# Kernel tuning notes

Hardware: AMD Instinct MI355X
Metric: run time of the kernel (lower is better)

The kernel has to match this reference:

```python
import jax, jax.numpy as jnp
import numpy as np

B, N, CC, CF, H, W = 4, 4, 256, 512, 128, 128
h, w = H // 2, W // 2


def _upsample2x(x):
    return jnp.repeat(jnp.repeat(x, 2, axis=2), 2, axis=3)


def setup_inputs() -> dict:
    key = jax.random.key(0)
    ks = jax.random.split(key, 8)
    return {
        "contexts": jax.random.normal(ks[0], (B, N, CC, H, W), dtype=jnp.float32),
        "mainstream": jax.random.normal(ks[1], (B, CF, h, w), dtype=jnp.float32),
        "Wc_w": jax.random.normal(ks[2], (CC, CC), dtype=jnp.float32) * 0.02,  # 1x1 conv Cc->Cc
        "Wc_b": jnp.zeros((CC,), dtype=jnp.float32),
        "Wf_w": jax.random.normal(ks[3], (CC, CF), dtype=jnp.float32) * 0.02,  # 1x1 conv Cf->Cc
        "Wf_b": jnp.zeros((CC,), dtype=jnp.float32),
        "Wv_w": jax.random.normal(ks[4], (CC, CF, 3, 3), dtype=jnp.float32) * 0.02,  # 3x3 conv Cf->Cc
        "Wv_b": jnp.zeros((CC,), dtype=jnp.float32),
    }


def reference(contexts, mainstream, Wc_w, Wc_b, Wf_w, Wf_b, Wv_w, Wv_b):
    # queries: 1x1 conv Cf->Cc on mainstream  [B,Cc,h,w]
    queries = jnp.einsum('oc,bchw->bohw', Wf_w, mainstream) + Wf_b[None, :, None, None]
    # keys: 1x1 conv Cc->Cc applied to every context  [B,N,Cc,H,W]
    keys = jnp.einsum('oc,bnchw->bnohw', Wc_w, contexts) + Wc_b[None, None, :, None, None]
    # values: 3x3 conv Cf->Cc, padding 1  [B,Cc,h,w]
    values = jax.lax.conv_general_dilated(
        mainstream, Wv_w, window_strides=(1, 1), padding='SAME',
        dimension_numbers=('NCHW', 'OIHW', 'NCHW')) + Wv_b[None, :, None, None]
    q_up = _upsample2x(queries)   # [B,Cc,H,W]
    v_up = _upsample2x(values)    # [B,Cc,H,W]
    # per-pixel attention scores over the N contexts
    scores = jnp.einsum('bnchw,bchw->bnhw', keys, q_up)      # [B,N,H,W]
    attn = jax.nn.softmax(scores, axis=1)                    # softmax over contexts
    attn_out = jnp.einsum('bnchw,bnhw->bchw', contexts, attn)
    return attn_out + v_up
```

## Files before the change

### kernel.cpp

```cpp
#include <hip/hip_runtime.h>

#define NB   4
#define NN   4
#define CCh  256
#define CFh  512
#define HH   128
#define WW   128
#define PLO  4096
#define PHI  16384

typedef __bf16 bf16;
typedef __bf16 bf16x8 __attribute__((ext_vector_type(8)));
typedef float  f32x4  __attribute__((ext_vector_type(4)));
typedef float  f32x2  __attribute__((ext_vector_type(2)));

__device__ __forceinline__ void gll16(const void* g, void* lds) {
    __builtin_amdgcn_global_load_lds(
        (const __attribute__((address_space(1))) void*)g,
        (__attribute__((address_space(3))) void*)lds, 16, 0, 0);
}

__device__ __forceinline__ unsigned pack2bf(float a, float b) {
    unsigned short ua = __builtin_bit_cast(unsigned short, (bf16)a);
    unsigned short ub = __builtin_bit_cast(unsigned short, (bf16)b);
    return (unsigned)ua | ((unsigned)ub << 16);
}

__global__ void prep_mqk(const float* __restrict__ Wc_w, const float* __restrict__ Wf_w,
                         const float* __restrict__ Wf_b, bf16* __restrict__ M_qk,
                         float* __restrict__ d_qk) {
    __shared__ float red[256];
    int c = blockIdx.y;
    int f = blockIdx.x * 256 + threadIdx.x;
    float s = 0.f;
#pragma unroll 8
    for (int o = 0; o < CCh; ++o)
        s += Wc_w[o * CCh + c] * Wf_w[o * CFh + f];
    M_qk[c * CFh + f] = (bf16)s;
    if (blockIdx.x == 0) {
        int o = threadIdx.x;
        red[o] = Wc_w[o * CCh + c] * Wf_b[o];
        __syncthreads();
        for (int st = 128; st > 0; st >>= 1) {
            if (threadIdx.x < st) red[threadIdx.x] += red[threadIdx.x + st];
            __syncthreads();
        }
        if (threadIdx.x == 0) d_qk[c] = red[0];
    }
}

__global__ void prep_ms(const float* __restrict__ ms, bf16* __restrict__ ms_t) {
    __shared__ float tile[32][33];
    int b = blockIdx.z;
    int p0 = blockIdx.x * 32, f0 = blockIdx.y * 32;
    int tx = threadIdx.x;
    int r = tx >> 5, cc = tx & 31;
    const float* src = ms + (size_t)b * CFh * PLO;
#pragma unroll
    for (int q = 0; q < 4; ++q) {
        int fl = q * 8 + r;
        tile[fl][cc] = src[(size_t)(f0 + fl) * PLO + p0 + cc];
    }
    __syncthreads();
    bf16* dst = ms_t + (size_t)b * PLO * CFh;
    int fp = tx & 15;
    int r2 = tx >> 4;
#pragma unroll
    for (int q = 0; q < 2; ++q) {
        int pl = q * 16 + r2;
        unsigned w = pack2bf(tile[2 * fp][pl], tile[2 * fp + 1][pl]);
        *((unsigned*)(dst + (size_t)(p0 + pl) * CFh + f0) + fp) = w;
    }
}

__global__ void prep_wv(const float* __restrict__ Wv_w, bf16* __restrict__ Wv_p,
                        bf16* __restrict__ zerob) {
    int tid = blockIdx.x * 256 + threadIdx.x;
    int t = tid / (CCh * CFh);
    int rem = tid % (CCh * CFh);
    int c = rem / CFh, f = rem % CFh;
    Wv_p[tid] = (bf16)Wv_w[(size_t)(c * CFh + f) * 9 + t];
    if (tid < 1024) zerob[tid] = (bf16)0.f;
}

__global__ __launch_bounds__(256) void gemm_kernel(
    const bf16* __restrict__ Wv_p,
    const bf16* __restrict__ M_qk,
    const bf16* __restrict__ ms_t,
    const float* __restrict__ d_qk,
    const bf16* __restrict__ zerob,
    float* __restrict__ v3, bf16* __restrict__ qk_out) {
    __shared__ __align__(16) bf16 Alds[128 * 32];
    __shared__ __align__(16) bf16 Blds[128 * 32];

    const int tx = threadIdx.x;
    const int wave = tx >> 6, lane = tx & 63;
    const int ptile = blockIdx.x, ctile = blockIdx.y;
    const int z = blockIdx.z;
    const int mode = (z >= 12);
    const int b = mode ? (z - 12) : (z / 3);
    const int tg = mode ? 0 : (z % 3);
    const int t0 = tg * 3;
    const int ntaps = mode ? 1 : 3;

    const bf16* Wbase = mode ? M_qk : (Wv_p + (size_t)t0 * CCh * CFh);
    const bf16* msb = ms_t + (size_t)b * PLO * CFh;

    int idx0 = wave * 2048 + lane * 16;
    int idx1 = idx0 + 1024;
    int rA0 = idx0 >> 6, fq0 = (idx0 >> 4) & 3;
    int rA1 = idx1 >> 6, fq1 = (idx1 >> 4) & 3;
    const size_t aoff0 = (size_t)(ctile * 128 + rA0) * CFh + fq0 * 8;
    const size_t aoff1 = (size_t)(ctile * 128 + rA1) * CFh + fq1 * 8;
    char* ldsA0 = (char*)Alds + wave * 2048;
    char* ldsA1 = ldsA0 + 1024;
    char* ldsB0 = (char*)Blds + wave * 2048;
    char* ldsB1 = ldsB0 + 1024;

    const int p0 = ptile * 128 + rA0, p1 = ptile * 128 + rA1;
    const int i0 = p0 >> 6, j0 = p0 & 63;
    const int i1 = p1 >> 6, j1 = p1 & 63;

    f32x4 acc[4][4];
#pragma unroll
    for (int mi = 0; mi < 4; ++mi)
#pragma unroll
        for (int ni = 0; ni < 4; ++ni) acc[mi][ni] = f32x4{0.f, 0.f, 0.f, 0.f};

    const int wm = wave >> 1, wn = wave & 1;
    const int quad = lane >> 4, l15 = lane & 15;

    for (int t = 0; t < ntaps; ++t) {
        const int dy = mode ? 0 : ((t0 + t) / 3 - 1);
        const int dx = mode ? 0 : ((t0 + t) % 3 - 1);
        const bf16* Wt = Wbase + (size_t)t * CCh * CFh;
        int si0 = i0 + dy, sj0 = j0 + dx, si1 = i1 + dy, sj1 = j1 + dx;
        bool ok0 = (unsigned)si0 < 64u && (unsigned)sj0 < 64u;
        bool ok1 = (unsigned)si1 < 64u && (unsigned)sj1 < 64u;
        const bf16* bsrc0 = ok0 ? msb + (size_t)(si0 * 64 + sj0) * CFh + fq0 * 8 : zerob;
        const bf16* bsrc1 = ok1 ? msb + (size_t)(si1 * 64 + sj1) * CFh + fq1 * 8 : zerob;

        for (int fc = 0; fc < CFh / 32; ++fc) {
            const int f0 = fc * 32;
            __syncthreads();
            gll16(Wt + aoff0 + f0, ldsA0);
            gll16(Wt + aoff1 + f0, ldsA1);
            gll16(bsrc0 + f0, ldsB0);
            gll16(bsrc1 + f0, ldsB1);
            __syncthreads();

            bf16x8 af[4], bfr[4];
#pragma unroll
            for (int mi = 0; mi < 4; ++mi)
                af[mi] = *(const bf16x8*)&Alds[(wm * 64 + mi * 16 + l15) * 32 + quad * 8];
#pragma unroll
            for (int ni = 0; ni < 4; ++ni)
                bfr[ni] = *(const bf16x8*)&Blds[(wn * 64 + ni * 16 + l15) * 32 + quad * 8];
#pragma unroll
            for (int mi = 0; mi < 4; ++mi)
#pragma unroll
                for (int ni = 0; ni < 4; ++ni)
                    acc[mi][ni] = __builtin_amdgcn_mfma_f32_16x16x32_bf16(
                        af[mi], bfr[ni], acc[mi][ni], 0, 0, 0);
        }
    }

    if (mode) {
        bf16* obase = qk_out + (size_t)b * CCh * PLO;
#pragma unroll
        for (int mi = 0; mi < 4; ++mi) {
            int cb = ctile * 128 + wm * 64 + mi * 16 + quad * 4;
#pragma unroll
            for (int ni = 0; ni < 4; ++ni) {
                int p = ptile * 128 + wn * 64 + ni * 16 + l15;
                bf16* op = obase + (size_t)cb * PLO + p;
#pragma unroll
                for (int r = 0; r < 4; ++r)
                    op[(size_t)r * PLO] = (bf16)(acc[mi][ni][r] + d_qk[cb + r]);
            }
        }
    } else {
        float* obase = v3 + (size_t)(tg * NB + b) * CCh * PLO;
#pragma unroll
        for (int mi = 0; mi < 4; ++mi) {
            int cb = ctile * 128 + wm * 64 + mi * 16 + quad * 4;
#pragma unroll
            for (int ni = 0; ni < 4; ++ni) {
                int p = ptile * 128 + wn * 64 + ni * 16 + l15;
                float* op = obase + (size_t)cb * PLO + p;
#pragma unroll
                for (int r = 0; r < 4; ++r)
                    op[(size_t)r * PLO] = acc[mi][ni][r];
            }
        }
    }
}

__global__ __launch_bounds__(512) void attn_kernel(
    const float* __restrict__ ctx,
    const bf16* __restrict__ qk,
    const float* __restrict__ v3,
    const float* __restrict__ Wv_b,
    float* __restrict__ out) {
    __shared__ f32x4 swred[4][8][16];
    const int tx = threadIdx.x;
    const int pq = tx & 15;
    const int cc = tx >> 4;
    const int lane = tx & 63;
    const int wv = tx >> 6;
    const int quad = lane >> 4;

    const int pbase = blockIdx.x << 6;
    const int b = pbase >> 14;
    const int rem = pbase & 16383;
    const int hh = rem >> 7;
    const int w0 = rem & 127;
    const int wq = w0 + pq * 4;
    const int i = hh >> 1, j0 = wq >> 1;

    const int c0 = cc * 8;
    const size_t NSTR = (size_t)CCh * PHI;
    const float* cbase = ctx + (size_t)b * NN * NSTR + (size_t)c0 * PHI
                             + (size_t)hh * WW + wq;
    const bf16* qkb = qk + ((size_t)b * CCh + c0) * PLO + i * 64 + j0;
    const float* vbp = v3 + ((size_t)b * CCh + c0) * PLO + i * 64 + j0;

    f32x4 vals[4][8];
    f32x4 s[4];
#pragma unroll
    for (int n = 0; n < 4; ++n) s[n] = f32x4{0.f, 0.f, 0.f, 0.f};

#pragma unroll
    for (int cj = 0; cj < 8; ++cj) {
        unsigned qw = *(const unsigned*)(qkb + (size_t)cj * PLO);
        float qa = __uint_as_float(qw << 16);
        float qb = __uint_as_float(qw & 0xffff0000u);
        f32x4 qv = {qa, qa, qb, qb};
#pragma unroll
        for (int n = 0; n < 4; ++n) {
            vals[n][cj] = *(const f32x4*)(cbase + n * NSTR + (size_t)cj * PHI);
            s[n] += vals[n][cj] * qv;
        }
    }
#pragma unroll
    for (int n = 0; n < 4; ++n) {
#pragma unroll
        for (int m = 16; m <= 32; m <<= 1) {
            f32x4 t;
            t[0] = __shfl_xor(s[n][0], m);
            t[1] = __shfl_xor(s[n][1], m);
            t[2] = __shfl_xor(s[n][2], m);
            t[3] = __shfl_xor(s[n][3], m);
            s[n] += t;
        }
    }
    f32x4 sq = (quad == 0) ? s[0] : (quad == 1) ? s[1] : (quad == 2) ? s[2] : s[3];
    swred[quad][wv][pq] = sq;
    __syncthreads();

    f32x4 t4[4];
#pragma unroll
    for (int n = 0; n < 4; ++n) {
        f32x4 a = swred[n][0][pq];
#pragma unroll
        for (int w = 1; w < 8; ++w) a += swred[n][w][pq];
        t4[n] = a;
    }
    f32x4 mx;
#pragma unroll
    for (int k = 0; k < 4; ++k)
        mx[k] = fmaxf(fmaxf(t4[0][k], t4[1][k]), fmaxf(t4[2][k], t4[3][k]));
    f32x4 e[4];
#pragma unroll
    for (int n = 0; n < 4; ++n)
#pragma unroll
        for (int k = 0; k < 4; ++k) e[n][k] = __expf(t4[n][k] - mx[k]);
    f32x4 ssum = e[0] + e[1] + e[2] + e[3];
    f32x4 a4[4];
#pragma unroll
    for (int n = 0; n < 4; ++n)
#pragma unroll
        for (int k = 0; k < 4; ++k) a4[n][k] = e[n][k] / ssum[k];

    float* outp = out + ((size_t)b * CCh + c0) * PHI + (size_t)hh * WW + wq;
#pragma unroll
    for (int cj = 0; cj < 8; ++cj) {
        f32x2 vv = *(const f32x2*)(vbp + (size_t)cj * PLO);
        vv += *(const f32x2*)(vbp + 4194304 + (size_t)cj * PLO);
        vv += *(const f32x2*)(vbp + 8388608 + (size_t)cj * PLO);
        float bc = Wv_b[c0 + cj];
        float va = vv[0] + bc, vb2 = vv[1] + bc;
        f32x4 o = vals[0][cj] * a4[0] + vals[1][cj] * a4[1] +
                  vals[2][cj] * a4[2] + vals[3][cj] * a4[3] +
                  f32x4{va, va, vb2, vb2};
        *(f32x4*)(outp + (size_t)cj * PHI) = o;
    }
}

extern "C" void kernel_launch(void* const* d_in, const int* in_sizes, int n_in,
                              void* d_out, int out_size, void* d_ws, size_t ws_size,
                              hipStream_t stream) {
    const float* ctx  = (const float*)d_in[0];
    const float* ms   = (const float*)d_in[1];
    const float* Wc_w = (const float*)d_in[2];
    const float* Wf_w = (const float*)d_in[4];
    const float* Wf_b = (const float*)d_in[5];
    const float* Wv_w = (const float*)d_in[6];
    const float* Wv_b = (const float*)d_in[7];
    float* out = (float*)d_out;

    char* ws = (char*)d_ws;
    bf16*  ms_t  = (bf16*)ws;
    bf16*  Wv_p  = (bf16*)(ws + 16777216);
    bf16*  M_qk  = (bf16*)(ws + 19136512);
    float* d_qk  = (float*)(ws + 19398656);
    bf16*  zerob = (bf16*)(ws + 19399680);
    bf16*  qk    = (bf16*)(ws + 19401728);
    float* v3    = (float*)(ws + 27790336);

    prep_mqk<<<dim3(2, 256), 256, 0, stream>>>(Wc_w, Wf_w, Wf_b, M_qk, d_qk);
    prep_ms<<<dim3(128, 16, 4), 256, 0, stream>>>(ms, ms_t);
    prep_wv<<<dim3(4608), 256, 0, stream>>>(Wv_w, Wv_p, zerob);
    gemm_kernel<<<dim3(32, 2, 16), 256, 0, stream>>>(Wv_p, M_qk, ms_t, d_qk,
                                                     zerob, v3, qk);
    attn_kernel<<<dim3(1024), 512, 0, stream>>>(ctx, qk, v3, Wv_b, out);
}
```

Before: 503.3 us.

## Double-buffer LDS tiles in the MFMA GEMM to overlap loads with compute

The nested tap and channel-chunk loops are flattened into a single iteration loop over double-buffered LDS tiles. The next chunk's global-to-LDS loads are issued before computing on the current buffer, using explicit vmcnt waits and barriers. This hides global memory latency behind MFMA work, at the cost of twice the LDS footprint and hand-managed waitcnt ordering that must stay correct.

Result: slower. 513.7 us (+2.1%).

```diff
diff --git a/kernel.cpp b/kernel.cpp
--- a/kernel.cpp
+++ b/kernel.cpp
@@ -90,8 +90,8 @@
     const float* __restrict__ d_qk,
     const bf16* __restrict__ zerob,
     float* __restrict__ v3, bf16* __restrict__ qk_out) {
-    __shared__ __align__(16) bf16 Alds[128 * 32];
-    __shared__ __align__(16) bf16 Blds[128 * 32];
+    __shared__ __align__(16) bf16 Alds[2][128 * 32];
+    __shared__ __align__(16) bf16 Blds[2][128 * 32];
 
     const int tx = threadIdx.x;
     const int wave = tx >> 6, lane = tx & 63;
@@ -101,7 +101,7 @@
     const int b = mode ? (z - 12) : (z / 3);
     const int tg = mode ? 0 : (z % 3);
     const int t0 = tg * 3;
-    const int ntaps = mode ? 1 : 3;
+    const int NIT = mode ? 16 : 48;
 
     const bf16* Wbase = mode ? M_qk : (Wv_p + (size_t)t0 * CCh * CFh);
     const bf16* msb = ms_t + (size_t)b * PLO * CFh;
@@ -112,10 +112,6 @@
     int rA1 = idx1 >> 6, fq1 = (idx1 >> 4) & 3;
     const size_t aoff0 = (size_t)(ctile * 128 + rA0) * CFh + fq0 * 8;
     const size_t aoff1 = (size_t)(ctile * 128 + rA1) * CFh + fq1 * 8;
-    char* ldsA0 = (char*)Alds + wave * 2048;
-    char* ldsA1 = ldsA0 + 1024;
-    char* ldsB0 = (char*)Blds + wave * 2048;
-    char* ldsB1 = ldsB0 + 1024;
 
     const int p0 = ptile * 128 + rA0, p1 = ptile * 128 + rA1;
     const int i0 = p0 >> 6, j0 = p0 & 63;
@@ -130,40 +126,72 @@
     const int wm = wave >> 1, wn = wave & 1;
     const int quad = lane >> 4, l15 = lane & 15;
 
-    for (int t = 0; t < ntaps; ++t) {
-        const int dy = mode ? 0 : ((t0 + t) / 3 - 1);
-        const int dx = mode ? 0 : ((t0 + t) % 3 - 1);
-        const bf16* Wt = Wbase + (size_t)t * CCh * CFh;
-        int si0 = i0 + dy, sj0 = j0 + dx, si1 = i1 + dy, sj1 = j1 + dx;
-        bool ok0 = (unsigned)si0 < 64u && (unsigned)sj0 < 64u;
-        bool ok1 = (unsigned)si1 < 64u && (unsigned)sj1 < 64u;
-        const bf16* bsrc0 = ok0 ? msb + (size_t)(si0 * 64 + sj0) * CFh + fq0 * 8 : zerob;
-        const bf16* bsrc1 = ok1 ? msb + (size_t)(si1 * 64 + sj1) * CFh + fq1 * 8 : zerob;
-
-        for (int fc = 0; fc < CFh / 32; ++fc) {
-            const int f0 = fc * 32;
-            __syncthreads();
-            gll16(Wt + aoff0 + f0, ldsA0);
-            gll16(Wt + aoff1 + f0, ldsA1);
-            gll16(bsrc0 + f0, ldsB0);
-            gll16(bsrc1 + f0, ldsB1);
-            __syncthreads();
-
-            bf16x8 af[4], bfr[4];
-#pragma unroll
-            for (int mi = 0; mi < 4; ++mi)
-                af[mi] = *(const bf16x8*)&Alds[(wm * 64 + mi * 16 + l15) * 32 + quad * 8];
+    const bf16* bsrc0; const bf16* bsrc1; const bf16* Wt;
+#define SET_TAP(tt) do {                                                        \
+        int t_ = (tt);                                                          \
+        int dy = mode ? 0 : ((t0 + t_) / 3 - 1);                                \
+        int dx = mode ? 0 : ((t0 + t_) % 3 - 1);                                \
+        int si0 = i0 + dy, sj0 = j0 + dx, si1 = i1 + dy, sj1 = j1 + dx;         \
+        bsrc0 = ((unsigned)si0 < 64u && (unsigned)sj0 < 64u)                    \
+                    ? msb + (size_t)(si0 * 64 + sj0) * CFh + fq0 * 8 : zerob;   \
+        bsrc1 = ((unsigned)si1 < 64u && (unsigned)sj1 < 64u)                    \
+                    ? msb + (size_t)(si1 * 64 + sj1) * CFh + fq1 * 8 : zerob;   \
+        Wt = Wbase + (size_t)t_ * CCh * CFh;                                    \
+    } while (0)
+
+    SET_TAP(0);
+    {
+        char* lA = (char*)(&Alds[0][0]) + wave * 2048;
+        char* lB = (char*)(&Blds[0][0]) + wave * 2048;
+        gll16(Wt + aoff0, lA);
+        gll16(Wt + aoff1, lA + 1024);
+        gll16(bsrc0, lB);
+        gll16(bsrc1, lB + 1024);
+    }
+    asm volatile("s_waitcnt vmcnt(0)" ::: "memory");
+    __builtin_amdgcn_s_barrier();
+    asm volatile("" ::: "memory");
+
+    for (int it = 0; it < NIT; ++it) {
+        const int buf = it & 1;
+        const int nx = it + 1;
+        if (nx < NIT) {
+            if ((nx & 15) == 0) SET_TAP(nx >> 4);
+            const int fo = (nx & 15) * 32;
+            char* lA = (char*)(&Alds[buf ^ 1][0]) + wave * 2048;
+            char* lB = (char*)(&Blds[buf ^ 1][0]) + wave * 2048;
+            gll16(Wt + aoff0 + fo, lA);
+            gll16(Wt + aoff1 + fo, lA + 1024);
+            gll16(bsrc0 + fo, lB);
+            gll16(bsrc1 + fo, lB + 1024);
+            asm volatile("s_waitcnt vmcnt(4)" ::: "memory");
+        } else {
+            asm volatile("s_waitcnt vmcnt(0)" ::: "memory");
+        }
+        __builtin_amdgcn_s_barrier();
+        asm volatile("" ::: "memory");
+
+        const bf16* Ab = &Alds[buf][0];
+        const bf16* Bb = &Blds[buf][0];
+        bf16x8 af[4], bfr[4];
+#pragma unroll
+        for (int mi = 0; mi < 4; ++mi)
+            af[mi] = *(const bf16x8*)&Ab[(wm * 64 + mi * 16 + l15) * 32 + quad * 8];
+#pragma unroll
+        for (int ni = 0; ni < 4; ++ni)
+            bfr[ni] = *(const bf16x8*)&Bb[(wn * 64 + ni * 16 + l15) * 32 + quad * 8];
+#pragma unroll
+        for (int mi = 0; mi < 4; ++mi)
 #pragma unroll
             for (int ni = 0; ni < 4; ++ni)
-                bfr[ni] = *(const bf16x8*)&Blds[(wn * 64 + ni * 16 + l15) * 32 + quad * 8];
-#pragma unroll
-            for (int mi = 0; mi < 4; ++mi)
-#pragma unroll
-                for (int ni = 0; ni < 4; ++ni)
-                    acc[mi][ni] = __builtin_amdgcn_mfma_f32_16x16x32_bf16(
-                        af[mi], bfr[ni], acc[mi][ni], 0, 0, 0);
-        }
-    }
+                acc[mi][ni] = __builtin_amdgcn_mfma_f32_16x16x32_bf16(
+                    af[mi], bfr[ni], acc[mi][ni], 0, 0, 0);
+
+        asm volatile("" ::: "memory");
+        __builtin_amdgcn_s_barrier();
+        asm volatile("" ::: "memory");
+    }
+#undef SET_TAP
 
     if (mode) {
         bf16* obase = qk_out + (size_t)b * CCh * PLO;
```

## Pad mainstream into halo grid and share B tile across three horizontal taps

Applied to the files above, without the earlier changes.

The transposed mainstream is now stored in a zero-padded 66x72 grid per batch, so conv taps need no bounds checks or zero buffer. The GEMM loads a two-row-plus-halo B strip once per K chunk and reuses it for all three dx taps by shifting the LDS read offset. The three tap weight tiles are loaded together, which cuts the number of barriers and global B reloads. The three prep kernels are merged into one launch, plus a memset of the padded buffer, at the cost of more LDS and extra memset traffic.

After: 491.5 us. 2.3% less time.

```diff
diff --git a/kernel.cpp b/kernel.cpp
--- a/kernel.cpp
+++ b/kernel.cpp
@@ -8,6 +8,9 @@
 #define WW   128
 #define PLO  4096
 #define PHI  16384
+#define GR   66
+#define GC   72
+#define PLANE_E (GR * GC * CFh)
 
 typedef __bf16 bf16;
 typedef __bf16 bf16x8 __attribute__((ext_vector_type(8)));
@@ -26,72 +29,71 @@
     return (unsigned)ua | ((unsigned)ub << 16);
 }
 
-__global__ void prep_mqk(const float* __restrict__ Wc_w, const float* __restrict__ Wf_w,
-                         const float* __restrict__ Wf_b, bf16* __restrict__ M_qk,
-                         float* __restrict__ d_qk) {
+__global__ void prep_fused(const float* __restrict__ Wc_w, const float* __restrict__ Wf_w,
+                           const float* __restrict__ Wf_b, const float* __restrict__ ms,
+                           const float* __restrict__ Wv_w,
+                           bf16* __restrict__ M_qk, float* __restrict__ d_qk,
+                           bf16* __restrict__ msg, bf16* __restrict__ Wv_p) {
     __shared__ float red[256];
-    int c = blockIdx.y;
-    int f = blockIdx.x * 256 + threadIdx.x;
-    float s = 0.f;
+    __shared__ float tile[32][33];
+    const int bid = blockIdx.x, tx = threadIdx.x;
+
+    if (bid < 512) {
+        int c = bid >> 1;
+        int f = (bid & 1) * 256 + tx;
+        float s = 0.f;
 #pragma unroll 8
-    for (int o = 0; o < CCh; ++o)
-        s += Wc_w[o * CCh + c] * Wf_w[o * CFh + f];
-    M_qk[c * CFh + f] = (bf16)s;
-    if (blockIdx.x == 0) {
-        int o = threadIdx.x;
-        red[o] = Wc_w[o * CCh + c] * Wf_b[o];
+        for (int o = 0; o < CCh; ++o)
+            s += Wc_w[o * CCh + c] * Wf_w[o * CFh + f];
+        M_qk[c * CFh + f] = (bf16)s;
+        if ((bid & 1) == 0) {
+            red[tx] = Wc_w[tx * CCh + c] * Wf_b[tx];
+            __syncthreads();
+            for (int st = 128; st > 0; st >>= 1) {
+                if (tx < st) red[tx] += red[tx + st];
+                __syncthreads();
+            }
+            if (tx == 0) d_qk[c] = red[0];
+        }
+    } else if (bid < 5120) {
+        int tid = (bid - 512) * 256 + tx;
+        int t = tid / (CCh * CFh);
+        int rem = tid % (CCh * CFh);
+        int c = rem / CFh, f = rem % CFh;
+        Wv_p[tid] = (bf16)Wv_w[(size_t)(c * CFh + f) * 9 + t];
+    } else {
+        int id2 = bid - 5120;
+        int x = id2 & 127, y = (id2 >> 7) & 15, b = id2 >> 11;
+        int p0 = x * 32, f0 = y * 32;
+        int r = tx >> 5, cc = tx & 31;
+        const float* src = ms + (size_t)b * CFh * PLO;
+#pragma unroll
+        for (int q = 0; q < 4; ++q) {
+            int fl = q * 8 + r;
+            tile[fl][cc] = src[(size_t)(f0 + fl) * PLO + p0 + cc];
+        }
         __syncthreads();
-        for (int st = 128; st > 0; st >>= 1) {
-            if (threadIdx.x < st) red[threadIdx.x] += red[threadIdx.x + st];
-            __syncthreads();
-        }
-        if (threadIdx.x == 0) d_qk[c] = red[0];
-    }
-}
-
-__global__ void prep_ms(const float* __restrict__ ms, bf16* __restrict__ ms_t) {
-    __shared__ float tile[32][33];
-    int b = blockIdx.z;
-    int p0 = blockIdx.x * 32, f0 = blockIdx.y * 32;
-    int tx = threadIdx.x;
-    int r = tx >> 5, cc = tx & 31;
-    const float* src = ms + (size_t)b * CFh * PLO;
-#pragma unroll
-    for (int q = 0; q < 4; ++q) {
-        int fl = q * 8 + r;
-        tile[fl][cc] = src[(size_t)(f0 + fl) * PLO + p0 + cc];
-    }
-    __syncthreads();
-    bf16* dst = ms_t + (size_t)b * PLO * CFh;
-    int fp = tx & 15;
-    int r2 = tx >> 4;
-#pragma unroll
-    for (int q = 0; q < 2; ++q) {
-        int pl = q * 16 + r2;
-        unsigned w = pack2bf(tile[2 * fp][pl], tile[2 * fp + 1][pl]);
-        *((unsigned*)(dst + (size_t)(p0 + pl) * CFh + f0) + fp) = w;
-    }
-}
-
-__global__ void prep_wv(const float* __restrict__ Wv_w, bf16* __restrict__ Wv_p,
-                        bf16* __restrict__ zerob) {
-    int tid = blockIdx.x * 256 + threadIdx.x;
-    int t = tid / (CCh * CFh);
-    int rem = tid % (CCh * CFh);
-    int c = rem / CFh, f = rem % CFh;
-    Wv_p[tid] = (bf16)Wv_w[(size_t)(c * CFh + f) * 9 + t];
-    if (tid < 1024) zerob[tid] = (bf16)0.f;
+        bf16* dstb = msg + (size_t)b * PLANE_E;
+        int fp = tx & 15, r2 = tx >> 4;
+#pragma unroll
+        for (int q = 0; q < 2; ++q) {
+            int pl = q * 16 + r2;
+            int pix = p0 + pl;
+            int pi = pix >> 6, pj = pix & 63;
+            unsigned w = pack2bf(tile[2 * fp][pl], tile[2 * fp + 1][pl]);
+            *((unsigned*)(dstb + ((size_t)(pi + 1) * GC + pj + 1) * CFh + f0) + fp) = w;
+        }
+    }
 }
 
 __global__ __launch_bounds__(256) void gemm_kernel(
     const bf16* __restrict__ Wv_p,
     const bf16* __restrict__ M_qk,
-    const bf16* __restrict__ ms_t,
+    const bf16* __restrict__ msg,
     const float* __restrict__ d_qk,
-    const bf16* __restrict__ zerob,
     float* __restrict__ v3, bf16* __restrict__ qk_out) {
-    __shared__ __align__(16) bf16 Alds[128 * 32];
-    __shared__ __align__(16) bf16 Blds[128 * 32];
+    __shared__ __align__(16) bf16 Alds[3 * 128 * 32];
+    __shared__ __align__(16) bf16 Blds[2 * GC * 32];
 
     const int tx = threadIdx.x;
     const int wave = tx >> 6, lane = tx & 63;
@@ -100,26 +102,30 @@
     const int mode = (z >= 12);
     const int b = mode ? (z - 12) : (z / 3);
     const int tg = mode ? 0 : (z % 3);
-    const int t0 = tg * 3;
+    const int dy = mode ? 0 : (tg - 1);
     const int ntaps = mode ? 1 : 3;
 
-    const bf16* Wbase = mode ? M_qk : (Wv_p + (size_t)t0 * CCh * CFh);
-    const bf16* msb = ms_t + (size_t)b * PLO * CFh;
-
-    int idx0 = wave * 2048 + lane * 16;
-    int idx1 = idx0 + 1024;
-    int rA0 = idx0 >> 6, fq0 = (idx0 >> 4) & 3;
-    int rA1 = idx1 >> 6, fq1 = (idx1 >> 4) & 3;
-    const size_t aoff0 = (size_t)(ctile * 128 + rA0) * CFh + fq0 * 8;
-    const size_t aoff1 = (size_t)(ctile * 128 + rA1) * CFh + fq1 * 8;
-    char* ldsA0 = (char*)Alds + wave * 2048;
-    char* ldsA1 = ldsA0 + 1024;
-    char* ldsB0 = (char*)Blds + wave * 2048;
-    char* ldsB1 = ldsB0 + 1024;
-
-    const int p0 = ptile * 128 + rA0, p1 = ptile * 128 + rA1;
-    const int i0 = p0 >> 6, j0 = p0 & 63;
-    const int i1 = p1 >> 6, j1 = p1 & 63;
+    const bf16* Wbase = mode ? M_qk : (Wv_p + (size_t)tg * 3 * CCh * CFh);
+    const bf16* msb = msg + (size_t)b * PLANE_E;
+    const int i0 = ptile * 2;
+
+    int aoffs[6];
+#pragma unroll
+    for (int k = 0; k < 6; ++k) {
+        int q = wave + 4 * k;
+        int tap = q >> 3, s = q & 7;
+        aoffs[k] = tap * (CCh * CFh) + (ctile * 128 + s * 16 + (lane >> 2)) * CFh
+                 + (lane & 3) * 8;
+    }
+    int boffs[3];
+#pragma unroll
+    for (int k = 0; k < 3; ++k) {
+        int q = wave + 4 * k;
+        int cfl = q * 16 + (lane >> 2);
+        int ri = (cfl >= GC) ? 1 : 0;
+        int jj = cfl - GC * ri;
+        boffs[k] = ((i0 + ri + dy + 1) * GC + jj) * CFh + (lane & 3) * 8;
+    }
 
     f32x4 acc[4][4];
 #pragma unroll
@@ -129,33 +135,35 @@
 
     const int wm = wave >> 1, wn = wave & 1;
     const int quad = lane >> 4, l15 = lane & 15;
-
-    for (int t = 0; t < ntaps; ++t) {
-        const int dy = mode ? 0 : ((t0 + t) / 3 - 1);
-        const int dx = mode ? 0 : ((t0 + t) % 3 - 1);
-        const bf16* Wt = Wbase + (size_t)t * CCh * CFh;
-        int si0 = i0 + dy, sj0 = j0 + dx, si1 = i1 + dy, sj1 = j1 + dx;
-        bool ok0 = (unsigned)si0 < 64u && (unsigned)sj0 < 64u;
-        bool ok1 = (unsigned)si1 < 64u && (unsigned)sj1 < 64u;
-        const bf16* bsrc0 = ok0 ? msb + (size_t)(si0 * 64 + sj0) * CFh + fq0 * 8 : zerob;
-        const bf16* bsrc1 = ok1 ? msb + (size_t)(si1 * 64 + sj1) * CFh + fq1 * 8 : zerob;
-
-        for (int fc = 0; fc < CFh / 32; ++fc) {
-            const int f0 = fc * 32;
-            __syncthreads();
-            gll16(Wt + aoff0 + f0, ldsA0);
-            gll16(Wt + aoff1 + f0, ldsA1);
-            gll16(bsrc0 + f0, ldsB0);
-            gll16(bsrc1 + f0, ldsB1);
-            __syncthreads();
-
+    const int nA = ntaps * 2;
+
+    for (int fc = 0; fc < 16; ++fc) {
+        const int f0 = fc * 32;
+        __syncthreads();
+#pragma unroll
+        for (int k = 0; k < 6; ++k)
+            if (k < nA)
+                gll16(Wbase + aoffs[k] + f0, (char*)Alds + (wave + 4 * k) * 1024);
+#pragma unroll
+        for (int k = 0; k < 3; ++k)
+            if (wave + 4 * k < 9)
+                gll16(msb + boffs[k] + f0, (char*)Blds + (wave + 4 * k) * 1024);
+        __syncthreads();
+
+        for (int t = 0; t < ntaps; ++t) {
+            const int dxo = mode ? 1 : t;
             bf16x8 af[4], bfr[4];
 #pragma unroll
             for (int mi = 0; mi < 4; ++mi)
-                af[mi] = *(const bf16x8*)&Alds[(wm * 64 + mi * 16 + l15) * 32 + quad * 8];
-#pragma unroll
-            for (int ni = 0; ni < 4; ++ni)
-                bfr[ni] = *(const bf16x8*)&Blds[(wn * 64 + ni * 16 + l15) * 32 + quad * 8];
+                af[mi] = *(const bf16x8*)((const char*)Alds + t * 8192 +
+                          (wm * 64 + mi * 16 + l15) * 64 + quad * 16);
+#pragma unroll
+            for (int ni = 0; ni < 4; ++ni) {
+                int pl = wn * 64 + ni * 16 + l15;
+                int ri = pl >> 6, j = pl & 63;
+                bfr[ni] = *(const bf16x8*)((const char*)Blds +
+                           (ri * GC + j + dxo) * 64 + quad * 16);
+            }
 #pragma unroll
             for (int mi = 0; mi < 4; ++mi)
 #pragma unroll
@@ -310,18 +318,16 @@
     float* out = (float*)d_out;
 
     char* ws = (char*)d_ws;
-    bf16*  ms_t  = (bf16*)ws;
-    bf16*  Wv_p  = (bf16*)(ws + 16777216);
-    bf16*  M_qk  = (bf16*)(ws + 19136512);
-    float* d_qk  = (float*)(ws + 19398656);
-    bf16*  zerob = (bf16*)(ws + 19399680);
-    bf16*  qk    = (bf16*)(ws + 19401728);
-    float* v3    = (float*)(ws + 27790336);
-
-    prep_mqk<<<dim3(2, 256), 256, 0, stream>>>(Wc_w, Wf_w, Wf_b, M_qk, d_qk);
-    prep_ms<<<dim3(128, 16, 4), 256, 0, stream>>>(ms, ms_t);
-    prep_wv<<<dim3(4608), 256, 0, stream>>>(Wv_w, Wv_p, zerob);
-    gemm_kernel<<<dim3(32, 2, 16), 256, 0, stream>>>(Wv_p, M_qk, ms_t, d_qk,
-                                                     zerob, v3, qk);
+    bf16*  msg  = (bf16*)ws;
+    bf16*  Wv_p = (bf16*)(ws + 19464192);
+    bf16*  M_qk = (bf16*)(ws + 21823488);
+    float* d_qk = (float*)(ws + 22085632);
+    bf16*  qk   = (bf16*)(ws + 22086656);
+    float* v3   = (float*)(ws + 30475264);
+
+    hipMemsetAsync(msg, 0, 19464192, stream);
+    prep_fused<<<dim3(13312), 256, 0, stream>>>(Wc_w, Wf_w, Wf_b, ms, Wv_w,
+                                                M_qk, d_qk, msg, Wv_p);
+    gemm_kernel<<<dim3(32, 2, 16), 256, 0, stream>>>(Wv_p, M_qk, msg, d_qk, v3, qk);
     attn_kernel<<<dim3(1024), 512, 0, stream>>>(ctx, qk, v3, Wv_b, out);
 }
```
